# Kernel optimization log

Hardware: AMD Instinct MI355X
Metric: run time of the kernel (lower is better)

## Reference

```python
import jax, jax.numpy as jnp
from jax import lax
import numpy as np

B, CIN, COUT, D, TDIM, E = 2, 16, 8, 96, 256, 8


def setup_inputs() -> dict:
    key = jax.random.key(0)
    ks = jax.random.split(key, 12)
    s = lambda fan: 1.0 / np.sqrt(fan)
    return {
        "x": jax.random.normal(ks[0], (B, CIN, D, D, D), jnp.float32),
        "text_features": jax.random.normal(ks[1], (B, TDIM), jnp.float32),
        # expert weight basis [E, Cout, Cin, 3, 3, 3] (kaiming-uniform-ish)
        "weight_basis": jax.random.uniform(ks[2], (E, COUT, CIN, 3, 3, 3), jnp.float32, -s(CIN * 27), s(CIN * 27)),
        "bias_basis": jnp.zeros((E, COUT), jnp.float32),
        # router MLP: text_dim -> 64 -> E
        "r_w1": jax.random.uniform(ks[3], (TDIM, 64), jnp.float32, -s(TDIM), s(TDIM)),
        "r_b1": jax.random.uniform(ks[4], (64,), jnp.float32, -s(TDIM), s(TDIM)),
        "r_w2": jax.random.uniform(ks[5], (64, E), jnp.float32, -s(64), s(64)),
        "r_b2": jax.random.uniform(ks[6], (E,), jnp.float32, -s(64), s(64)),
        # modulator MLP: text_dim -> 64 -> Cout
        "m_w1": jax.random.uniform(ks[7], (TDIM, 64), jnp.float32, -s(TDIM), s(TDIM)),
        "m_b1": jax.random.uniform(ks[8], (64,), jnp.float32, -s(TDIM), s(TDIM)),
        "m_w2": jax.random.uniform(ks[9], (64, COUT), jnp.float32, -s(64), s(64)),
        "m_b2": jax.random.uniform(ks[10], (COUT,), jnp.float32, -s(64), s(64)),
    }


def reference(x, text_features, weight_basis, bias_basis,
              r_w1, r_b1, r_w2, r_b2, m_w1, m_b1, m_w2, m_b2):
    b, cin = x.shape[0], x.shape[1]
    cout = weight_basis.shape[1]
    # router -> softmax routing weights over experts
    h = jax.nn.leaky_relu(text_features @ r_w1 + r_b1, 0.1)
    router_logits = h @ r_w2 + r_b2                      # [b, E]
    routing_weights = jax.nn.softmax(router_logits, -1)  # [b, E]
    # modulator -> per-sample channel gates
    g = jax.nn.leaky_relu(text_features @ m_w1 + m_b1, 0.1)
    gamma = jax.nn.sigmoid(g @ m_w2 + m_b2)              # [b, Cout]
    # per-sample dynamic conv weights via expert mixing
    cw = jnp.einsum('be,eoixyz->boixyz', routing_weights, weight_basis)  # [b,Cout,Cin,3,3,3]
    cb = routing_weights @ bias_basis                                    # [b, Cout]
    # grouped-conv trick: batch folded into channels, groups=b
    xr = x.reshape(1, b * cin, *x.shape[2:])
    wr = cw.reshape(b * cout, cin, 3, 3, 3)
    out = lax.conv_general_dilated(
        xr, wr, window_strides=(1, 1, 1), padding=[(1, 1)] * 3,
        dimension_numbers=('NCDHW', 'OIDHW', 'NCDHW'), feature_group_count=b)
    out = out.reshape(b, cout, *out.shape[2:]) + cb[:, :, None, None, None]
    out = out * (1.0 + gamma[:, :, None, None, None])
    return out, router_logits, routing_weights
```

## Files before the change

kernel.cpp:

```cpp
#include <hip/hip_runtime.h>
#include <math.h>

#define NB 2
#define CIN 16
#define COUT 8
#define DD 96
#define TDIM 256
#define NE 8
#define VOX (DD*DD*DD)
#define OUT_ELEMS (NB*COUT*VOX)

#define XT_BYTES ((size_t)NB * VOX * 32)
#define WS_A_F 7168
#define WS_D_F 7184

#define LX 18
#define PLANE (LX*LX)
#define NVX (PLANE*5)
#define HALFB (NVX*16)

#define NTB3 (VOX/512)
#define MWN (COUT*CIN*27)

#define CONV_BLOCKS (36*32*NB)

typedef _Float16 f16x8 __attribute__((ext_vector_type(8)));
typedef float f32x4 __attribute__((ext_vector_type(4)));

__global__ __launch_bounds__(256) void transpose_setup(
    const float* __restrict__ x, _Float16* __restrict__ xt,
    const float* __restrict__ text,
    const float* __restrict__ wb,
    const float* __restrict__ bb,
    const float* __restrict__ rw1, const float* __restrict__ rb1,
    const float* __restrict__ rw2, const float* __restrict__ rb2,
    const float* __restrict__ mw1, const float* __restrict__ mb1,
    const float* __restrict__ mw2, const float* __restrict__ mb2,
    float* __restrict__ dout_tail,
    char* __restrict__ tab)
{
    __shared__ struct {
        float mw[MWN];
        float part[256];
        float hg[2][64];
        float logits[NE];
        float rwv[NE];
    } s;
    const int t = threadIdx.x;
    const int b = blockIdx.y;

    if (blockIdx.x == 0) {
        __builtin_amdgcn_s_setprio(1);
        {
            const int o = t & 127;
            const int which = o >> 6, j = o & 63;
            const int kh = t >> 7;
            const float* __restrict__ w1 = which ? mw1 : rw1;
            const float* __restrict__ tx = text + b*TDIM + kh*128;
            const float* __restrict__ wp = w1 + (size_t)(kh*128)*64 + j;
            float a0 = 0.f, a1 = 0.f, a2 = 0.f, a3 = 0.f;
            #pragma unroll 8
            for (int k = 0; k < 128; k += 4) {
                a0 = fmaf(tx[k+0], wp[(k+0)*64], a0);
                a1 = fmaf(tx[k+1], wp[(k+1)*64], a1);
                a2 = fmaf(tx[k+2], wp[(k+2)*64], a2);
                a3 = fmaf(tx[k+3], wp[(k+3)*64], a3);
            }
            s.part[t] = (a0 + a1) + (a2 + a3);
        }
        __syncthreads();
        if (t < 128) {
            const int which = t >> 6, j = t & 63;
            float acc = (which ? mb1 : rb1)[j] + s.part[t] + s.part[t + 128];
            s.hg[which][j] = (acc >= 0.f) ? acc : 0.1f * acc;
        }
        __syncthreads();
        if (t < NE) {
            float acc = rb2[t];
            #pragma unroll
            for (int k = 0; k < 64; ++k) acc = fmaf(s.hg[0][k], rw2[k*NE + t], acc);
            s.logits[t] = acc;
            dout_tail[b*NE + t] = acc;
        }
        __syncthreads();
        if (t < NE) {
            float mx = s.logits[0];
            for (int k = 1; k < NE; ++k) mx = fmaxf(mx, s.logits[k]);
            float ssum = 0.f;
            for (int k = 0; k < NE; ++k) ssum += expf(s.logits[k] - mx);
            const float w = expf(s.logits[t] - mx) / ssum;
            s.rwv[t] = w;
            dout_tail[NB*NE + b*NE + t] = w;
        }
        __syncthreads();
        float rv[NE];
        #pragma unroll
        for (int e = 0; e < NE; ++e) rv[e] = s.rwv[e];

        if (t < COUT) {
            float acc = mb2[t];
            #pragma unroll
            for (int k = 0; k < 64; ++k) acc = fmaf(s.hg[1][k], mw2[k*COUT + t], acc);
            const float gamma = 1.f / (1.f + expf(-acc));
            const float a = 1.f + gamma;
            float cb = 0.f;
            #pragma unroll
            for (int e = 0; e < NE; ++e) cb = fmaf(rv[e], bb[e*COUT + t], cb);
            ((float*)tab)[WS_A_F + b*COUT + t] = a;
            ((float*)tab)[WS_D_F + b*COUT + t] = cb * a;
        }

        #pragma unroll
        for (int i0 = 0; i0 < (MWN + 255)/256; ++i0) {
            const int i = i0*256 + t;
            if (i < MWN) {
                float v = 0.f;
                #pragma unroll
                for (int e = 0; e < NE; ++e) v = fmaf(rv[e], wb[e*MWN + i], v);
                s.mw[i] = v;
            }
        }
        __syncthreads();

        for (int r = t; r < 14*64*8; r += 256) {
            const int c  = r >> 9;
            const int l  = (r >> 3) & 63;
            const int j  = r & 7;
            const int q  = l >> 4;
            const int n  = l & 15;
            const int p  = q & 1;
            const int ci = (q >> 1)*8 + j;
            int tap;
            if (c < 9)        tap = (c/3)*9 + (c%3)*3 + p;
            else if (c < 12)  tap = (c-9)*9 + p*3 + 2;
            else if (c == 12) tap = p*9 + 8;
            else              tap = p ? -1 : 26;
            float v = 0.f;
            if (n < 8 && tap >= 0) v = s.mw[(n*CIN + ci)*27 + tap];
            ((_Float16*)tab)[b*7168 + r] = (_Float16)v;
        }
        __builtin_amdgcn_s_setprio(0);
        return;
    }

    const int vh = (blockIdx.x - 1) * 256 + t;
    const float* __restrict__ xb = x + (size_t)b * CIN * VOX;

    float2 f[CIN];
    #pragma unroll
    for (int ci = 0; ci < CIN; ++ci)
        f[ci] = ((const float2*)(xb + (size_t)ci * VOX))[vh];

    union { _Float16 h[16]; uint4 u[2]; } o0, o1;
    #pragma unroll
    for (int ci = 0; ci < CIN; ++ci) {
        o0.h[ci] = (_Float16)f[ci].x;
        o1.h[ci] = (_Float16)f[ci].y;
    }
    uint4* __restrict__ dst = (uint4*)(xt + (size_t)b * VOX * 16) + (size_t)vh * 4;
    dst[0] = o0.u[0];
    dst[1] = o0.u[1];
    dst[2] = o1.u[0];
    dst[3] = o1.u[1];
}

__global__ __launch_bounds__(256) void conv_mfma(
    const _Float16* __restrict__ xt,
    const char* __restrict__ tab,
    float* __restrict__ out)
{
    __shared__ char lds[2*HALFB];
    const int tid  = threadIdx.x;
    const int lane = tid & 63;
    const int wv   = tid >> 6;

    const int nid = (blockIdx.x & 7) * (CONV_BLOCKS/8) + (blockIdx.x >> 3);
    const int bx  = nid % 36;
    const int by  = (nid / 36) % 32;
    const int b   = nid / (36*32);

    const int z0   = by * 3;
    const int xti  = bx % 6;
    const int yti  = bx / 6;
    const int x0   = xti * 16, y0 = yti * 16;

    const f16x8* __restrict__ bfp = (const f16x8*)tab;
    f16x8 bfrag[14];
    #pragma unroll
    for (int c = 0; c < 14; ++c)
        bfrag[c] = bfp[(b*14 + c)*64 + lane];

    const _Float16* __restrict__ xtb = xt + (size_t)b * VOX * 16;
    for (int sv = tid; sv < NVX; sv += 256) {
        const int lz = sv / PLANE;
        const int r1 = sv - lz * PLANE;
        const int ly = r1 / LX;
        const int lx = r1 - ly * LX;
        const int zg = z0 - 1 + lz, yg = y0 - 1 + ly, xg = x0 - 1 + lx;
        const bool ok = ((unsigned)zg < 96u) & ((unsigned)yg < 96u) & ((unsigned)xg < 96u);
        const int zc = ok ? zg : 0, yc = ok ? yg : 0, xc = ok ? xg : 0;
        const uint4* __restrict__ p = (const uint4*)(xtb + (size_t)((zc*DD + yc)*DD + xc) * 16);
        uint4 lo = {0,0,0,0}, hi = {0,0,0,0};
        if (ok) { lo = p[0]; hi = p[1]; }
        *(uint4*)&lds[sv*16]         = lo;
        *(uint4*)&lds[HALFB + sv*16] = hi;
    }
    __syncthreads();

    const int q    = lane >> 4;
    const int m    = lane & 15;
    const int pbit = q & 1;
    const int hbit = q >> 1;

    const float* tabf = (const float*)tab;
    const float a_n = tabf[WS_A_F + b*8 + (m & 7)];
    const float d_n = tabf[WS_D_F + b*8 + (m & 7)];

    const int com = hbit*HALFB + m*16;
    const int dA = pbit*16;
    const int dB = pbit*288;
    const int dC = pbit*5184;

    #define LD_A(p_, dy_)  (*(const f16x8*)&lds[((p_)*PLANE + (yi+(dy_))*LX)*16 + com + dA])
    #define LD_G(p_)       (*(const f16x8*)&lds[((p_)*PLANE + yi*LX + 2)*16 + com + dB])
    #define LD_H12(zi_)    (*(const f16x8*)&lds[((zi_)*PLANE + (yi+2)*LX + 2)*16 + com + dC])
    #define LD_H13(zi_)    (*(const f16x8*)&lds[(((zi_)+2)*PLANE + (yi+2)*LX + 2)*16 + com])

    #pragma unroll
    for (int yi4 = 0; yi4 < 4; ++yi4) {
        const int yi = wv*4 + yi4;

        f16x8 A[3][3], G[3];
        #pragma unroll
        for (int dy = 0; dy < 3; ++dy) { A[0][dy] = LD_A(0, dy); A[1][dy] = LD_A(1, dy); }
        G[0] = LD_G(0); G[1] = LD_G(1);

        #pragma unroll
        for (int zi = 0; zi < 3; ++zi) {
            #pragma unroll
            for (int dy = 0; dy < 3; ++dy) A[2][dy] = LD_A(zi+2, dy);
            G[2] = LD_G(zi+2);
            const f16x8 H12v = LD_H12(zi);
            const f16x8 H13v = LD_H13(zi);

            f32x4 acc0 = {0.f,0.f,0.f,0.f}, acc1 = {0.f,0.f,0.f,0.f};
            acc0 = __builtin_amdgcn_mfma_f32_16x16x32_f16(A[0][0], bfrag[0],  acc0, 0,0,0);
            acc1 = __builtin_amdgcn_mfma_f32_16x16x32_f16(A[0][1], bfrag[1],  acc1, 0,0,0);
            acc0 = __builtin_amdgcn_mfma_f32_16x16x32_f16(A[0][2], bfrag[2],  acc0, 0,0,0);
            acc1 = __builtin_amdgcn_mfma_f32_16x16x32_f16(A[1][0], bfrag[3],  acc1, 0,0,0);
            acc0 = __builtin_amdgcn_mfma_f32_16x16x32_f16(A[1][1], bfrag[4],  acc0, 0,0,0);
            acc1 = __builtin_amdgcn_mfma_f32_16x16x32_f16(A[1][2], bfrag[5],  acc1, 0,0,0);
            acc0 = __builtin_amdgcn_mfma_f32_16x16x32_f16(A[2][0], bfrag[6],  acc0, 0,0,0);
            acc1 = __builtin_amdgcn_mfma_f32_16x16x32_f16(A[2][1], bfrag[7],  acc1, 0,0,0);
            acc0 = __builtin_amdgcn_mfma_f32_16x16x32_f16(A[2][2], bfrag[8],  acc0, 0,0,0);
            acc1 = __builtin_amdgcn_mfma_f32_16x16x32_f16(G[0],    bfrag[9],  acc1, 0,0,0);
            acc0 = __builtin_amdgcn_mfma_f32_16x16x32_f16(G[1],    bfrag[10], acc0, 0,0,0);
            acc1 = __builtin_amdgcn_mfma_f32_16x16x32_f16(G[2],    bfrag[11], acc1, 0,0,0);
            acc0 = __builtin_amdgcn_mfma_f32_16x16x32_f16(H12v,    bfrag[12], acc0, 0,0,0);
            acc1 = __builtin_amdgcn_mfma_f32_16x16x32_f16(H13v,    bfrag[13], acc1, 0,0,0);

            if (m < 8) {
                const int zz = z0 + zi, yy = y0 + yi;
                float* __restrict__ op = out + (size_t)(b*COUT + m)*VOX
                                            + (size_t)(zz*DD + yy)*DD + x0 + q*4;
                f32x4 res;
                #pragma unroll
                for (int r = 0; r < 4; ++r) res[r] = fmaf(acc0[r] + acc1[r], a_n, d_n);
                *reinterpret_cast<f32x4*>(op) = res;
            }

            #pragma unroll
            for (int dy = 0; dy < 3; ++dy) { A[0][dy] = A[1][dy]; A[1][dy] = A[2][dy]; }
            G[0] = G[1]; G[1] = G[2];
        }
    }
    #undef LD_A
    #undef LD_G
    #undef LD_H12
    #undef LD_H13
}

extern "C" void kernel_launch(void* const* d_in, const int* in_sizes, int n_in,
                              void* d_out, int out_size, void* d_ws, size_t ws_size,
                              hipStream_t stream) {
    const float* x    = (const float*)d_in[0];
    const float* text = (const float*)d_in[1];
    const float* wb   = (const float*)d_in[2];
    const float* bb   = (const float*)d_in[3];
    const float* rw1  = (const float*)d_in[4];
    const float* rb1  = (const float*)d_in[5];
    const float* rw2  = (const float*)d_in[6];
    const float* rb2  = (const float*)d_in[7];
    const float* mw1  = (const float*)d_in[8];
    const float* mb1  = (const float*)d_in[9];
    const float* mw2  = (const float*)d_in[10];
    const float* mb2  = (const float*)d_in[11];

    float* out = (float*)d_out;
    _Float16* xt = (_Float16*)d_ws;
    char* tab = (char*)d_ws + XT_BYTES;

    transpose_setup<<<dim3(NTB3 + 1, NB), 256, 0, stream>>>(
        x, xt, text, wb, bb, rw1, rb1, rw2, rb2, mw1, mb1, mw2, mb2,
        out + OUT_ELEMS, tab);

    conv_mfma<<<dim3(CONV_BLOCKS), 256, 0, stream>>>(xt, tab, out);
}
```

Before: 235.0 us.

## Move router/weight-mixing setup to last-finishing transpose blocks via atomic counter

Removes the dedicated setup block and has every transpose block increment a global atomic counter after its work. The last two blocks to finish each compute the router MLP, softmax, modulator, and mixed conv weight table for one sample. The aim is to stop the serial setup block from sitting on the kernel's critical path alongside the transpose. This adds a memset launch and an atomic per block. Setup work now starts only after all other transposes finish, so it could lengthen the tail.

```diff
diff --git a/kernel.cpp b/kernel.cpp
--- a/kernel.cpp
+++ b/kernel.cpp
@@ -13,6 +13,7 @@
 #define XT_BYTES ((size_t)NB * VOX * 32)
 #define WS_A_F 7168
 #define WS_D_F 7184
+#define CTR_OFF 30720
 
 #define LX 18
 #define PLANE (LX*LX)
@@ -20,6 +21,7 @@
 #define HALFB (NVX*16)
 
 #define NTB3 (VOX/512)
+#define TOTB (NTB3*NB)
 #define MWN (COUT*CIN*27)
 
 #define CONV_BLOCKS (36*32*NB)
@@ -46,122 +48,130 @@
         float logits[NE];
         float rwv[NE];
     } s;
+    __shared__ int sdone;
     const int t = threadIdx.x;
     const int b = blockIdx.y;
 
-    if (blockIdx.x == 0) {
-        __builtin_amdgcn_s_setprio(1);
-        {
-            const int o = t & 127;
-            const int which = o >> 6, j = o & 63;
-            const int kh = t >> 7;
-            const float* __restrict__ w1 = which ? mw1 : rw1;
-            const float* __restrict__ tx = text + b*TDIM + kh*128;
-            const float* __restrict__ wp = w1 + (size_t)(kh*128)*64 + j;
-            float a0 = 0.f, a1 = 0.f, a2 = 0.f, a3 = 0.f;
-            #pragma unroll 8
-            for (int k = 0; k < 128; k += 4) {
-                a0 = fmaf(tx[k+0], wp[(k+0)*64], a0);
-                a1 = fmaf(tx[k+1], wp[(k+1)*64], a1);
-                a2 = fmaf(tx[k+2], wp[(k+2)*64], a2);
-                a3 = fmaf(tx[k+3], wp[(k+3)*64], a3);
-            }
-            s.part[t] = (a0 + a1) + (a2 + a3);
+    {
+        const int vh = blockIdx.x * 256 + t;
+        const float* __restrict__ xb = x + (size_t)b * CIN * VOX;
+
+        float2 f[CIN];
+        #pragma unroll
+        for (int ci = 0; ci < CIN; ++ci)
+            f[ci] = ((const float2*)(xb + (size_t)ci * VOX))[vh];
+
+        union { _Float16 h[16]; uint4 u[2]; } o0, o1;
+        #pragma unroll
+        for (int ci = 0; ci < CIN; ++ci) {
+            o0.h[ci] = (_Float16)f[ci].x;
+            o1.h[ci] = (_Float16)f[ci].y;
         }
-        __syncthreads();
-        if (t < 128) {
-            const int which = t >> 6, j = t & 63;
-            float acc = (which ? mb1 : rb1)[j] + s.part[t] + s.part[t + 128];
-            s.hg[which][j] = (acc >= 0.f) ? acc : 0.1f * acc;
+        uint4* __restrict__ dst = (uint4*)(xt + (size_t)b * VOX * 16) + (size_t)vh * 4;
+        dst[0] = o0.u[0];
+        dst[1] = o0.u[1];
+        dst[2] = o1.u[0];
+        dst[3] = o1.u[1];
+    }
+
+    __syncthreads();
+    if (t == 0)
+        sdone = (int)atomicAdd((unsigned*)(tab + CTR_OFF), 1u);
+    __syncthreads();
+    const int done = sdone;
+    if (done < TOTB - 2) return;
+    const int sb = done - (TOTB - 2);
+
+    __builtin_amdgcn_s_setprio(1);
+    {
+        const int o = t & 127;
+        const int which = o >> 6, j = o & 63;
+        const int kh = t >> 7;
+        const float* __restrict__ w1 = which ? mw1 : rw1;
+        const float* __restrict__ tx = text + sb*TDIM + kh*128;
+        const float* __restrict__ wp = w1 + (size_t)(kh*128)*64 + j;
+        float a0 = 0.f, a1 = 0.f, a2 = 0.f, a3 = 0.f;
+        #pragma unroll 8
+        for (int k = 0; k < 128; k += 4) {
+            a0 = fmaf(tx[k+0], wp[(k+0)*64], a0);
+            a1 = fmaf(tx[k+1], wp[(k+1)*64], a1);
+            a2 = fmaf(tx[k+2], wp[(k+2)*64], a2);
+            a3 = fmaf(tx[k+3], wp[(k+3)*64], a3);
         }
-        __syncthreads();
-        if (t < NE) {
-            float acc = rb2[t];
+        s.part[t] = (a0 + a1) + (a2 + a3);
+    }
+    __syncthreads();
+    if (t < 128) {
+        const int which = t >> 6, j = t & 63;
+        float acc = (which ? mb1 : rb1)[j] + s.part[t] + s.part[t + 128];
+        s.hg[which][j] = (acc >= 0.f) ? acc : 0.1f * acc;
+    }
+    __syncthreads();
+    if (t < NE) {
+        float acc = rb2[t];
+        #pragma unroll
+        for (int k = 0; k < 64; ++k) acc = fmaf(s.hg[0][k], rw2[k*NE + t], acc);
+        s.logits[t] = acc;
+        dout_tail[sb*NE + t] = acc;
+    }
+    __syncthreads();
+    if (t < NE) {
+        float mx = s.logits[0];
+        for (int k = 1; k < NE; ++k) mx = fmaxf(mx, s.logits[k]);
+        float ssum = 0.f;
+        for (int k = 0; k < NE; ++k) ssum += expf(s.logits[k] - mx);
+        const float w = expf(s.logits[t] - mx) / ssum;
+        s.rwv[t] = w;
+        dout_tail[NB*NE + sb*NE + t] = w;
+    }
+    __syncthreads();
+    float rv[NE];
+    #pragma unroll
+    for (int e = 0; e < NE; ++e) rv[e] = s.rwv[e];
+
+    if (t < COUT) {
+        float acc = mb2[t];
+        #pragma unroll
+        for (int k = 0; k < 64; ++k) acc = fmaf(s.hg[1][k], mw2[k*COUT + t], acc);
+        const float gamma = 1.f / (1.f + expf(-acc));
+        const float a = 1.f + gamma;
+        float cb = 0.f;
+        #pragma unroll
+        for (int e = 0; e < NE; ++e) cb = fmaf(rv[e], bb[e*COUT + t], cb);
+        ((float*)tab)[WS_A_F + sb*COUT + t] = a;
+        ((float*)tab)[WS_D_F + sb*COUT + t] = cb * a;
+    }
+
+    #pragma unroll
+    for (int i0 = 0; i0 < (MWN + 255)/256; ++i0) {
+        const int i = i0*256 + t;
+        if (i < MWN) {
+            float v = 0.f;
             #pragma unroll
-            for (int k = 0; k < 64; ++k) acc = fmaf(s.hg[0][k], rw2[k*NE + t], acc);
-            s.logits[t] = acc;
-            dout_tail[b*NE + t] = acc;
+            for (int e = 0; e < NE; ++e) v = fmaf(rv[e], wb[e*MWN + i], v);
+            s.mw[i] = v;
         }
-        __syncthreads();
-        if (t < NE) {
-            float mx = s.logits[0];
-            for (int k = 1; k < NE; ++k) mx = fmaxf(mx, s.logits[k]);
-            float ssum = 0.f;
-            for (int k = 0; k < NE; ++k) ssum += expf(s.logits[k] - mx);
-            const float w = expf(s.logits[t] - mx) / ssum;
-            s.rwv[t] = w;
-            dout_tail[NB*NE + b*NE + t] = w;
-        }
-        __syncthreads();
-        float rv[NE];
-        #pragma unroll
-        for (int e = 0; e < NE; ++e) rv[e] = s.rwv[e];
-
-        if (t < COUT) {
-            float acc = mb2[t];
-            #pragma unroll
-            for (int k = 0; k < 64; ++k) acc = fmaf(s.hg[1][k], mw2[k*COUT + t], acc);
-            const float gamma = 1.f / (1.f + expf(-acc));
-            const float a = 1.f + gamma;
-            float cb = 0.f;
-            #pragma unroll
-            for (int e = 0; e < NE; ++e) cb = fmaf(rv[e], bb[e*COUT + t], cb);
-            ((float*)tab)[WS_A_F + b*COUT + t] = a;
-            ((float*)tab)[WS_D_F + b*COUT + t] = cb * a;
-        }
-
-        #pragma unroll
-        for (int i0 = 0; i0 < (MWN + 255)/256; ++i0) {
-            const int i = i0*256 + t;
-            if (i < MWN) {
-                float v = 0.f;
-                #pragma unroll
-                for (int e = 0; e < NE; ++e) v = fmaf(rv[e], wb[e*MWN + i], v);
-                s.mw[i] = v;
-            }
-        }
-        __syncthreads();
-
-        for (int r = t; r < 14*64*8; r += 256) {
-            const int c  = r >> 9;
-            const int l  = (r >> 3) & 63;
-            const int j  = r & 7;
-            const int q  = l >> 4;
-            const int n  = l & 15;
-            const int p  = q & 1;
-            const int ci = (q >> 1)*8 + j;
-            int tap;
-            if (c < 9)        tap = (c/3)*9 + (c%3)*3 + p;
-            else if (c < 12)  tap = (c-9)*9 + p*3 + 2;
-            else if (c == 12) tap = p*9 + 8;
-            else              tap = p ? -1 : 26;
-            float v = 0.f;
-            if (n < 8 && tap >= 0) v = s.mw[(n*CIN + ci)*27 + tap];
-            ((_Float16*)tab)[b*7168 + r] = (_Float16)v;
-        }
-        __builtin_amdgcn_s_setprio(0);
-        return;
-    }
-
-    const int vh = (blockIdx.x - 1) * 256 + t;
-    const float* __restrict__ xb = x + (size_t)b * CIN * VOX;
-
-    float2 f[CIN];
-    #pragma unroll
-    for (int ci = 0; ci < CIN; ++ci)
-        f[ci] = ((const float2*)(xb + (size_t)ci * VOX))[vh];
-
-    union { _Float16 h[16]; uint4 u[2]; } o0, o1;
-    #pragma unroll
-    for (int ci = 0; ci < CIN; ++ci) {
-        o0.h[ci] = (_Float16)f[ci].x;
-        o1.h[ci] = (_Float16)f[ci].y;
-    }
-    uint4* __restrict__ dst = (uint4*)(xt + (size_t)b * VOX * 16) + (size_t)vh * 4;
-    dst[0] = o0.u[0];
-    dst[1] = o0.u[1];
-    dst[2] = o1.u[0];
-    dst[3] = o1.u[1];
+    }
+    __syncthreads();
+
+    for (int r = t; r < 14*64*8; r += 256) {
+        const int c  = r >> 9;
+        const int l  = (r >> 3) & 63;
+        const int j  = r & 7;
+        const int q  = l >> 4;
+        const int n  = l & 15;
+        const int p  = q & 1;
+        const int ci = (q >> 1)*8 + j;
+        int tap;
+        if (c < 9)        tap = (c/3)*9 + (c%3)*3 + p;
+        else if (c < 12)  tap = (c-9)*9 + p*3 + 2;
+        else if (c == 12) tap = p*9 + 8;
+        else              tap = p ? -1 : 26;
+        float v = 0.f;
+        if (n < 8 && tap >= 0) v = s.mw[(n*CIN + ci)*27 + tap];
+        ((_Float16*)tab)[sb*7168 + r] = (_Float16)v;
+    }
+    __builtin_amdgcn_s_setprio(0);
 }
 
 __global__ __launch_bounds__(256) void conv_mfma(
@@ -300,7 +310,9 @@
     _Float16* xt = (_Float16*)d_ws;
     char* tab = (char*)d_ws + XT_BYTES;
 
-    transpose_setup<<<dim3(NTB3 + 1, NB), 256, 0, stream>>>(
+    hipMemsetAsync(tab + CTR_OFF, 0, 4, stream);
+
+    transpose_setup<<<dim3(NTB3, NB), 256, 0, stream>>>(
         x, xt, text, wb, bb, rw1, rb1, rw2, rb2, mw1, mb1, mw2, mb2,
         out + OUT_ELEMS, tab);
 
```

Measured after the change: 253.7 us. +8.0%, slower.
